# Performance work log

Measured on AMD Instinct MI355X. Metric: run time of the kernel, lower is better.

Reference implementation:

```python
import jax, jax.numpy as jnp
import numpy as np
from jax import lax

L = 15      # time_conv_size
STRIDE = 2


def setup_inputs() -> dict:
    key = jax.random.key(0)
    k1, k2, k3 = jax.random.split(key, 3)
    x = jax.random.normal(k1, (8, 4096, 64), dtype=jnp.float32)
    w1 = jax.random.normal(k2, (L,), dtype=jnp.float32)
    w2 = jax.random.normal(k3, (L,), dtype=jnp.float32)
    return {"x": x, "w1": w1, "w2": w2}


def reference(x, w1, w2):
    # x: [B, T, C]; w1, w2: [L]
    B, T, C = x.shape
    p = L // 2
    # --- weighted local mean: mu[b,t,c] = sum_k w1[k] * x_pad[b,t+k,c] ---
    x_pad = jnp.pad(x, ((0, 0), (p, p), (0, 0)))
    mu = sum(w1[k] * x_pad[:, k:k + T, :] for k in range(L))  # [B,T,C]
    # --- centered diagonal bilinear (covariance) pooling ---
    xc_pad = jnp.pad(x - mu, ((0, 0), (p, p), (0, 0)))  # [B, T+2p, C]
    # strided window indices: I = ceil(T/STRIDE) windows of length L
    starts = jnp.arange(0, T, STRIDE)                   # [I]
    idx = starts[:, None] + jnp.arange(L)[None, :]      # [I, L]
    win = xc_pad[:, idx, :]                             # [B, I, L, C]
    sigma = jnp.einsum('bilc,l,bild->bicd', win, w2, win)
    I = starts.shape[0]
    sigma = sigma.reshape(B, I, C * C)
    mu_s = mu[:, ::STRIDE, :]                           # [B, I, C]
    out = jnp.concatenate([mu_s, sigma], axis=-1)       # [B, I, C + C*C]
    # K.l2_normalize over last axis (epsilon=1e-12)
    denom = lax.rsqrt(jnp.maximum(jnp.sum(out * out, axis=-1, keepdims=True), 1e-12))
    return out * denom
```

## Files before the change

### kernel.cpp

```cpp
#include <hip/hip_runtime.h>

#define Tdim 4096
#define Bdim 8
#define Cdim 64
#define Ldim 15
#define Idim 2048
#define OUTW 4160
#define G    4
#define RX   (2*G + 27)
#define RXC  (2*G + 13)

__global__ __launch_bounds__(256, 4) void cbp_kernel(const float* __restrict__ x,
                                                     const float* __restrict__ w1,
                                                     const float* __restrict__ w2,
                                                     float* __restrict__ out) {
    __shared__ float xbuf[RX][64];
    __shared__ float xcs[RXC][64];
    __shared__ float mus[G][64];
    __shared__ float red[4][G];
    __shared__ float scale_s[G];

    const int tid = threadIdx.x;
    const int blk = blockIdx.x;
    const int b  = blk >> 9;
    const int i0 = (blk & 511) << 2;
    const int s0 = i0 << 1;

    const float* xb = x + (size_t)b * (Tdim * Cdim);
    for (int v = tid; v < RX * 16; v += 256) {
        const int r  = v >> 4;
        const int c4 = (v & 15) << 2;
        const int t  = s0 - 14 + r;
        float4 val = make_float4(0.f, 0.f, 0.f, 0.f);
        if (t >= 0 && t < Tdim) val = *(const float4*)(xb + (size_t)t * Cdim + c4);
        *(float4*)(&xbuf[r][c4]) = val;
    }
    __syncthreads();

    for (int v = tid; v < RXC * 16; v += 256) {
        const int j  = v >> 4;
        const int c4 = (v & 15) << 2;
        const int t  = s0 - 7 + j;
        float4 m = make_float4(0.f, 0.f, 0.f, 0.f);
#pragma unroll
        for (int k = 0; k < Ldim; ++k) {
            const float w = w1[k];
            const float4 xv = *(const float4*)(&xbuf[j + k][c4]);
            m.x = fmaf(w, xv.x, m.x);
            m.y = fmaf(w, xv.y, m.y);
            m.z = fmaf(w, xv.z, m.z);
            m.w = fmaf(w, xv.w, m.w);
        }
        const float4 xv = *(const float4*)(&xbuf[j + 7][c4]);
        float4 xc = make_float4(0.f, 0.f, 0.f, 0.f);
        if (t >= 0 && t < Tdim)
            xc = make_float4(xv.x - m.x, xv.y - m.y, xv.z - m.z, xv.w - m.w);
        *(float4*)(&xcs[j][c4]) = xc;
        if (j >= 7 && j <= 13 && ((j - 7) & 1) == 0)
            *(float4*)(&mus[(j - 7) >> 1][c4]) = m;
    }
    __syncthreads();

    const int c0 = (tid >> 4) << 2;
    const int d0 = (tid & 15) << 2;
    float acc[G][4][4];
#pragma unroll
    for (int g = 0; g < G; ++g)
#pragma unroll
        for (int cc = 0; cc < 4; ++cc)
#pragma unroll
            for (int dd = 0; dd < 4; ++dd) acc[g][cc][dd] = 0.f;

#pragma unroll
    for (int r = 0; r < RXC; ++r) {
        const float4 xd = *(const float4*)(&xcs[r][d0]);
        const float4 xc = *(const float4*)(&xcs[r][c0]);
#pragma unroll
        for (int g = 0; g < G; ++g) {
            const int l = r - 2 * g;
            if (l >= 0 && l < Ldim) {
                const float w  = w2[l];
                const float a0 = w * xc.x, a1 = w * xc.y, a2 = w * xc.z, a3 = w * xc.w;
                acc[g][0][0] = fmaf(a0, xd.x, acc[g][0][0]);
                acc[g][0][1] = fmaf(a0, xd.y, acc[g][0][1]);
                acc[g][0][2] = fmaf(a0, xd.z, acc[g][0][2]);
                acc[g][0][3] = fmaf(a0, xd.w, acc[g][0][3]);
                acc[g][1][0] = fmaf(a1, xd.x, acc[g][1][0]);
                acc[g][1][1] = fmaf(a1, xd.y, acc[g][1][1]);
                acc[g][1][2] = fmaf(a1, xd.z, acc[g][1][2]);
                acc[g][1][3] = fmaf(a1, xd.w, acc[g][1][3]);
                acc[g][2][0] = fmaf(a2, xd.x, acc[g][2][0]);
                acc[g][2][1] = fmaf(a2, xd.y, acc[g][2][1]);
                acc[g][2][2] = fmaf(a2, xd.z, acc[g][2][2]);
                acc[g][2][3] = fmaf(a2, xd.w, acc[g][2][3]);
                acc[g][3][0] = fmaf(a3, xd.x, acc[g][3][0]);
                acc[g][3][1] = fmaf(a3, xd.y, acc[g][3][1]);
                acc[g][3][2] = fmaf(a3, xd.z, acc[g][3][2]);
                acc[g][3][3] = fmaf(a3, xd.w, acc[g][3][3]);
            }
        }
    }

    float local[G];
#pragma unroll
    for (int g = 0; g < G; ++g) {
        float s = 0.f;
#pragma unroll
        for (int cc = 0; cc < 4; ++cc)
#pragma unroll
            for (int dd = 0; dd < 4; ++dd) s = fmaf(acc[g][cc][dd], acc[g][cc][dd], s);
        local[g] = s;
    }
    if (tid < Cdim) {
#pragma unroll
        for (int g = 0; g < G; ++g) local[g] = fmaf(mus[g][tid], mus[g][tid], local[g]);
    }
#pragma unroll
    for (int off = 32; off; off >>= 1)
#pragma unroll
        for (int g = 0; g < G; ++g) local[g] += __shfl_down(local[g], off, 64);
    if ((tid & 63) == 0) {
        const int w = tid >> 6;
#pragma unroll
        for (int g = 0; g < G; ++g) red[w][g] = local[g];
    }
    __syncthreads();
    if (tid < G) {
        const float ss = red[0][tid] + red[1][tid] + red[2][tid] + red[3][tid];
        scale_s[tid] = rsqrtf(fmaxf(ss, 1e-12f));
    }
    __syncthreads();

#pragma unroll
    for (int g = 0; g < G; ++g) {
        const float sc = scale_s[g];
        float* orow = out + (size_t)(b * Idim + i0 + g) * OUTW;
        if (tid < 16) {
            float4 m4 = *(const float4*)(&mus[g][tid << 2]);
            m4.x *= sc; m4.y *= sc; m4.z *= sc; m4.w *= sc;
            *(float4*)(orow + (tid << 2)) = m4;
        }
        float* osig = orow + Cdim;
#pragma unroll
        for (int cc = 0; cc < 4; ++cc) {
            const float4 v = make_float4(acc[g][cc][0] * sc, acc[g][cc][1] * sc,
                                         acc[g][cc][2] * sc, acc[g][cc][3] * sc);
            *(float4*)(osig + (c0 + cc) * Cdim + d0) = v;
        }
    }
}

extern "C" void kernel_launch(void* const* d_in, const int* in_sizes, int n_in,
                              void* d_out, int out_size, void* d_ws, size_t ws_size,
                              hipStream_t stream) {
    const float* x  = (const float*)d_in[0];
    const float* w1 = (const float*)d_in[1];
    const float* w2 = (const float*)d_in[2];
    float* out = (float*)d_out;
    cbp_kernel<<<dim3(Bdim * (Idim / G)), dim3(256), 0, stream>>>(x, w1, w2, out);
}
```

Before: 287.2 us.

## Process output windows sequentially to cut registers, raise occupancy, use nontemporal stores

Restructures the covariance loop so each of the 4 windows is accumulated, reduced, normalized and stored one at a time. Only 16 accumulators are live instead of 64, and the launch bounds rise to 6 blocks per CU. Output writes become nontemporal stores, which suits the large streaming output. The trade-off is that shared-memory rows are reloaded per window rather than reused across windows, and there is now one block barrier per window.

```diff
diff --git a/kernel.cpp b/kernel.cpp
--- a/kernel.cpp
+++ b/kernel.cpp
@@ -10,15 +10,16 @@
 #define RX   (2*G + 27)
 #define RXC  (2*G + 13)
 
-__global__ __launch_bounds__(256, 4) void cbp_kernel(const float* __restrict__ x,
+typedef float v4f __attribute__((ext_vector_type(4)));
+
+__global__ __launch_bounds__(256, 6) void cbp_kernel(const float* __restrict__ x,
                                                      const float* __restrict__ w1,
                                                      const float* __restrict__ w2,
                                                      float* __restrict__ out) {
     __shared__ float xbuf[RX][64];
     __shared__ float xcs[RXC][64];
     __shared__ float mus[G][64];
-    __shared__ float red[4][G];
-    __shared__ float scale_s[G];
+    __shared__ float red[G][4];
 
     const int tid = threadIdx.x;
     const int blk = blockIdx.x;
@@ -63,89 +64,69 @@
 
     const int c0 = (tid >> 4) << 2;
     const int d0 = (tid & 15) << 2;
-    float acc[G][4][4];
+
 #pragma unroll
-    for (int g = 0; g < G; ++g)
+    for (int g = 0; g < G; ++g) {
+        float acc[4][4];
 #pragma unroll
         for (int cc = 0; cc < 4; ++cc)
 #pragma unroll
-            for (int dd = 0; dd < 4; ++dd) acc[g][cc][dd] = 0.f;
+            for (int dd = 0; dd < 4; ++dd) acc[cc][dd] = 0.f;
 
 #pragma unroll
-    for (int r = 0; r < RXC; ++r) {
-        const float4 xd = *(const float4*)(&xcs[r][d0]);
-        const float4 xc = *(const float4*)(&xcs[r][c0]);
-#pragma unroll
-        for (int g = 0; g < G; ++g) {
-            const int l = r - 2 * g;
-            if (l >= 0 && l < Ldim) {
-                const float w  = w2[l];
-                const float a0 = w * xc.x, a1 = w * xc.y, a2 = w * xc.z, a3 = w * xc.w;
-                acc[g][0][0] = fmaf(a0, xd.x, acc[g][0][0]);
-                acc[g][0][1] = fmaf(a0, xd.y, acc[g][0][1]);
-                acc[g][0][2] = fmaf(a0, xd.z, acc[g][0][2]);
-                acc[g][0][3] = fmaf(a0, xd.w, acc[g][0][3]);
-                acc[g][1][0] = fmaf(a1, xd.x, acc[g][1][0]);
-                acc[g][1][1] = fmaf(a1, xd.y, acc[g][1][1]);
-                acc[g][1][2] = fmaf(a1, xd.z, acc[g][1][2]);
-                acc[g][1][3] = fmaf(a1, xd.w, acc[g][1][3]);
-                acc[g][2][0] = fmaf(a2, xd.x, acc[g][2][0]);
-                acc[g][2][1] = fmaf(a2, xd.y, acc[g][2][1]);
-                acc[g][2][2] = fmaf(a2, xd.z, acc[g][2][2]);
-                acc[g][2][3] = fmaf(a2, xd.w, acc[g][2][3]);
-                acc[g][3][0] = fmaf(a3, xd.x, acc[g][3][0]);
-                acc[g][3][1] = fmaf(a3, xd.y, acc[g][3][1]);
-                acc[g][3][2] = fmaf(a3, xd.z, acc[g][3][2]);
-                acc[g][3][3] = fmaf(a3, xd.w, acc[g][3][3]);
-            }
+        for (int l = 0; l < Ldim; ++l) {
+            const int r = 2 * g + l;
+            const float4 xd = *(const float4*)(&xcs[r][d0]);
+            const float4 xc = *(const float4*)(&xcs[r][c0]);
+            const float w  = w2[l];
+            const float a0 = w * xc.x, a1 = w * xc.y, a2 = w * xc.z, a3 = w * xc.w;
+            acc[0][0] = fmaf(a0, xd.x, acc[0][0]);
+            acc[0][1] = fmaf(a0, xd.y, acc[0][1]);
+            acc[0][2] = fmaf(a0, xd.z, acc[0][2]);
+            acc[0][3] = fmaf(a0, xd.w, acc[0][3]);
+            acc[1][0] = fmaf(a1, xd.x, acc[1][0]);
+            acc[1][1] = fmaf(a1, xd.y, acc[1][1]);
+            acc[1][2] = fmaf(a1, xd.z, acc[1][2]);
+            acc[1][3] = fmaf(a1, xd.w, acc[1][3]);
+            acc[2][0] = fmaf(a2, xd.x, acc[2][0]);
+            acc[2][1] = fmaf(a2, xd.y, acc[2][1]);
+            acc[2][2] = fmaf(a2, xd.z, acc[2][2]);
+            acc[2][3] = fmaf(a2, xd.w, acc[2][3]);
+            acc[3][0] = fmaf(a3, xd.x, acc[3][0]);
+            acc[3][1] = fmaf(a3, xd.y, acc[3][1]);
+            acc[3][2] = fmaf(a3, xd.z, acc[3][2]);
+            acc[3][3] = fmaf(a3, xd.w, acc[3][3]);
         }
-    }
 
-    float local[G];
-#pragma unroll
-    for (int g = 0; g < G; ++g) {
-        float s = 0.f;
+        float ss = 0.f;
 #pragma unroll
         for (int cc = 0; cc < 4; ++cc)
 #pragma unroll
-            for (int dd = 0; dd < 4; ++dd) s = fmaf(acc[g][cc][dd], acc[g][cc][dd], s);
-        local[g] = s;
-    }
-    if (tid < Cdim) {
+            for (int dd = 0; dd < 4; ++dd) ss = fmaf(acc[cc][dd], acc[cc][dd], ss);
+        if (tid < Cdim) {
+            const float m = mus[g][tid];
+            ss = fmaf(m, m, ss);
+        }
 #pragma unroll
-        for (int g = 0; g < G; ++g) local[g] = fmaf(mus[g][tid], mus[g][tid], local[g]);
-    }
-#pragma unroll
-    for (int off = 32; off; off >>= 1)
-#pragma unroll
-        for (int g = 0; g < G; ++g) local[g] += __shfl_down(local[g], off, 64);
-    if ((tid & 63) == 0) {
-        const int w = tid >> 6;
-#pragma unroll
-        for (int g = 0; g < G; ++g) red[w][g] = local[g];
-    }
-    __syncthreads();
-    if (tid < G) {
-        const float ss = red[0][tid] + red[1][tid] + red[2][tid] + red[3][tid];
-        scale_s[tid] = rsqrtf(fmaxf(ss, 1e-12f));
-    }
-    __syncthreads();
+        for (int off = 32; off; off >>= 1) ss += __shfl_down(ss, off, 64);
+        if ((tid & 63) == 0) red[g][tid >> 6] = ss;
+        __syncthreads();
 
-#pragma unroll
-    for (int g = 0; g < G; ++g) {
-        const float sc = scale_s[g];
+        const float sstot = red[g][0] + red[g][1] + red[g][2] + red[g][3];
+        const float sc = rsqrtf(fmaxf(sstot, 1e-12f));
+
         float* orow = out + (size_t)(b * Idim + i0 + g) * OUTW;
         if (tid < 16) {
-            float4 m4 = *(const float4*)(&mus[g][tid << 2]);
-            m4.x *= sc; m4.y *= sc; m4.z *= sc; m4.w *= sc;
-            *(float4*)(orow + (tid << 2)) = m4;
+            const float4 m4 = *(const float4*)(&mus[g][tid << 2]);
+            v4f mv = { m4.x * sc, m4.y * sc, m4.z * sc, m4.w * sc };
+            __builtin_nontemporal_store(mv, (v4f*)(orow + (tid << 2)));
         }
         float* osig = orow + Cdim;
 #pragma unroll
         for (int cc = 0; cc < 4; ++cc) {
-            const float4 v = make_float4(acc[g][cc][0] * sc, acc[g][cc][1] * sc,
-                                         acc[g][cc][2] * sc, acc[g][cc][3] * sc);
-            *(float4*)(osig + (c0 + cc) * Cdim + d0) = v;
+            v4f v = { acc[cc][0] * sc, acc[cc][1] * sc,
+                      acc[cc][2] * sc, acc[cc][3] * sc };
+            __builtin_nontemporal_store(v, (v4f*)(osig + (c0 + cc) * Cdim + d0));
         }
     }
 }
```

Measured after the change: 332.4 us. +15.7%, slower.
